# Optimization experiments

Measured on AMD Instinct MI355X. Metric: run time of the kernel, lower is better.

## Reference

```python
import jax, jax.numpy as jnp
import numpy as np

D_MODEL = 768
NUM_HEADS = 12
D_K = D_MODEL // NUM_HEADS


def setup_inputs() -> dict:
    key = jax.random.key(0)
    ks = jax.random.split(key, 9)
    B, N, C = 32, 577, D_MODEL
    s = 1.0 / np.sqrt(C)
    x = jax.random.normal(ks[0], (B, N, C), dtype=jnp.float32)
    Wq = jax.random.normal(ks[1], (C, C), dtype=jnp.float32) * s
    bq = jnp.zeros((C,), dtype=jnp.float32)
    Wk = jax.random.normal(ks[2], (C, C), dtype=jnp.float32) * s
    bk = jnp.zeros((C,), dtype=jnp.float32)
    Wv = jax.random.normal(ks[3], (C, C), dtype=jnp.float32) * s
    bv = jnp.zeros((C,), dtype=jnp.float32)
    Wo = jax.random.normal(ks[4], (C, C), dtype=jnp.float32) * s
    bo = jnp.zeros((C,), dtype=jnp.float32)
    return {"x": x, "Wq": Wq, "bq": bq, "Wk": Wk, "bk": bk,
            "Wv": Wv, "bv": bv, "Wo": Wo, "bo": bo}


def reference(x, Wq, bq, Wk, bk, Wv, bv, Wo, bo):
    B, N, C = x.shape
    H, dk = NUM_HEADS, D_K
    # Linear projections (torch Linear: x @ W.T + b)
    q = (x @ Wq.T + bq).reshape(B, N, H, dk).transpose(0, 2, 1, 3)  # [B,H,N,dk]
    k = (x @ Wk.T + bk).reshape(B, N, H, dk).transpose(0, 2, 1, 3)
    v = (x @ Wv.T + bv).reshape(B, N, H, dk).transpose(0, 2, 1, 3)
    scale = 1.0 / jnp.sqrt(jnp.asarray(dk, dtype=x.dtype))
    scores = jnp.einsum('bhnd,bhmd->bhnm', q, k) * scale  # [B,H,N,N]
    attn = jax.nn.softmax(scores, axis=-1)
    out = jnp.einsum('bhnm,bhmd->bhnd', attn, v)  # [B,H,N,dk]
    out = out.transpose(0, 2, 1, 3).reshape(B, N, C)
    return out @ Wo.T + bo
```

## Files before the change

### kernel.cpp

```cpp
#include <hip/hip_runtime.h>
#include <cstdint>
#include <cstddef>

typedef float  f32x4   __attribute__((ext_vector_type(4)));
typedef __bf16 bf16x8  __attribute__((ext_vector_type(8)));
typedef short  short8  __attribute__((ext_vector_type(8)));
typedef short  short4v __attribute__((ext_vector_type(4)));
typedef float  float4v __attribute__((ext_vector_type(4)));

#define DEVI __device__ __forceinline__

constexpr int Bb = 32, Nn = 577, Cc = 768, Hh = 12, DK = 64;
constexpr int Mm   = Bb * Nn;
constexpr int NQKV = 3 * Cc;
constexpr int NKPAD = 640;
constexpr int NT = 10;
#define QSCALE 0.1803368926f

DEVI short f2bf(float f) {
  __bf16 h = (__bf16)f;
  short s;
  __builtin_memcpy(&s, &h, 2);
  return s;
}

DEVI void gload16(const short* g, short* l) {
  __builtin_amdgcn_global_load_lds(
      (const __attribute__((address_space(1))) void*)g,
      (__attribute__((address_space(3))) void*)l, 16, 0, 0);
}

DEVI f32x4 mfma16(bf16x8 a, bf16x8 b, f32x4 c) {
  return __builtin_amdgcn_mfma_f32_16x16x32_bf16(a, b, c, 0, 0, 0);
}

DEVI void remap_grouped(int bid, int nbm, int nbn, int GM, int& bm, int& bn) {
  const int nwg = nbm * nbn;
  const int xcd = bid & 7, j = bid >> 3;
  const int q = nwg >> 3, r = nwg & 7;
  int wg = (xcd < r ? xcd * (q + 1) : r * (q + 1) + (xcd - r) * q) + j;
  const int per = GM * nbn;
  int grp = wg / per;
  int first = grp * GM;
  int sz = min(GM, nbm - first);
  int rem = wg - grp * per;
  bm = first + rem % sz;
  bn = rem / sz;
}


__global__ void k_cvt_all(const float* __restrict__ x,
                          const float* __restrict__ Wq, const float* __restrict__ Wk,
                          const float* __restrict__ Wv, const float* __restrict__ Wo,
                          short* __restrict__ xb, short* __restrict__ wqkv,
                          short* __restrict__ wob) {
  const int NX4   = Mm * Cc / 4;
  const int WSZ4  = Cc * Cc / 4;
  int i = blockIdx.x * 256 + threadIdx.x;
  const float* src;
  short* dst;
  int e;
  if (i < NX4) { src = x; dst = xb; e = i; }
  else {
    int j = i - NX4;
    if (j < WSZ4)          { src = Wq; dst = wqkv;                e = j; }
    else if (j < 2 * WSZ4) { src = Wk; dst = wqkv + WSZ4 * 4;     e = j - WSZ4; }
    else if (j < 3 * WSZ4) { src = Wv; dst = wqkv + 2 * WSZ4 * 4; e = j - 2 * WSZ4; }
    else if (j < 4 * WSZ4) { src = Wo; dst = wob;                 e = j - 3 * WSZ4; }
    else return;
  }
  float4v v = *(const float4v*)(src + (size_t)e * 4);
  short4v o;
#pragma unroll
  for (int t = 0; t < 4; ++t) o[t] = f2bf(v[t]);
  *(short4v*)(dst + (size_t)e * 4) = o;
}

#define WAITV(N) asm volatile("s_waitcnt vmcnt(" #N ")" ::: "memory")

#define GPH(BUF, KK, MH, STAGE, WAIT)                                      \
  {                                                                        \
    const short* Ab_ = Al + (BUF) * 16384;                                 \
    const short* Bb_ = Bl + (BUF) * 16384;                                 \
    bf16x8 af_[4];                                                         \
    _Pragma("unroll")                                                      \
    for (int m_ = 0; m_ < 4; ++m_)                                         \
      af_[m_] = *(const bf16x8*)(Ab_ + (offA[(MH) * 4 + m_] ^ ((KK) * 32))); \
    if ((MH) == 0) {                                                       \
      _Pragma("unroll")                                                    \
      for (int n_ = 0; n_ < 4; ++n_)                                       \
        bfr[n_] = *(const bf16x8*)(Bb_ + (offB[n_] ^ ((KK) * 32)));        \
    }                                                                      \
    STAGE;                                                                 \
    WAIT;                                                                  \
    __builtin_amdgcn_s_barrier();                                          \
    __builtin_amdgcn_s_setprio(1);                                         \
    _Pragma("unroll")                                                      \
    for (int m_ = 0; m_ < 4; ++m_)                                         \
      _Pragma("unroll")                                                    \
      for (int n_ = 0; n_ < 4; ++n_)                                       \
        acc[(MH) * 4 + m_][n_] = mfma16(af_[m_], bfr[n_], acc[(MH) * 4 + m_][n_]); \
    __builtin_amdgcn_s_setprio(0);                                         \
    __builtin_amdgcn_s_barrier();                                          \
  }

DEVI void gemm256b(const short* __restrict__ A, const short* __restrict__ Bm,
                   int arows, int bm, int bn,
                   short* Al, short* Bl, f32x4 acc[8][4]) {
  const int tid = threadIdx.x;
  const int lane = tid & 63, w = tid >> 6;
  const int wm = w >> 2, wn = w & 3;
  const int qi = lane & 15, g = lane >> 4;

#pragma unroll
  for (int m = 0; m < 8; ++m)
#pragma unroll
    for (int n = 0; n < 4; ++n) acc[m][n] = (f32x4)0.0f;

  const int rloc = tid >> 3, c8 = tid & 7;
  const int gswz = (c8 ^ (rloc & 7)) * 8;
  const short* pA[4];
  const short* pB[4];
#pragma unroll
  for (int s = 0; s < 4; ++s) {
    int ra = bm * 256 + s * 64 + rloc; if (ra > arows - 1) ra = arows - 1;
    pA[s] = A  + (size_t)ra * Cc + gswz;
    pB[s] = Bm + (size_t)(bn * 256 + s * 64 + rloc) * Cc + gswz;
  }
  auto stA = [&](int buf, int s, int co) {
    gload16(pA[s] + co, Al + buf * 16384 + s * 4096 + tid * 8);
  };
  auto stB = [&](int buf, int s, int co) {
    gload16(pB[s] + co, Bl + buf * 16384 + s * 4096 + tid * 8);
  };

  int offA[8], offB[4];
#pragma unroll
  for (int m = 0; m < 8; ++m) {
    int r = wm * 128 + m * 16 + qi;
    offA[m] = r * 64 + ((g ^ (r & 7)) * 8);
  }
#pragma unroll
  for (int n = 0; n < 4; ++n) {
    int r = wn * 64 + n * 16 + qi;
    offB[n] = r * 64 + ((g ^ (r & 7)) * 8);
  }
  bf16x8 bfr[4];

  stA(0, 0, 0); stA(0, 1, 0); stA(0, 2, 0); stA(0, 3, 0);
  stB(0, 0, 0); stB(0, 1, 0); stB(0, 2, 0); stB(0, 3, 0);
  stB(1, 0, 64); stB(1, 1, 64);
  WAITV(2);
  __builtin_amdgcn_s_barrier();

#pragma unroll 1
  for (int i = 0; i < 5; ++i) {
    const int cb1  = 64 + 128 * i;
    const int cb0n = cb1 + 64;
    const int cb1n = cb1 + 128;
    GPH(0, 0, 0, (stB(1, 2, cb1),  stB(1, 3, cb1)),  (void)0);
    GPH(0, 0, 1, (stA(1, 0, cb1),  stA(1, 2, cb1)),  (void)0);
    GPH(0, 1, 0, (stA(1, 1, cb1),  stA(1, 3, cb1)),  (void)0);
    GPH(0, 1, 1, (stA(0, 0, cb0n), stA(0, 2, cb0n)), WAITV(4));
    GPH(1, 0, 0, (stA(0, 1, cb0n), stA(0, 3, cb0n)), WAITV(4));
    GPH(1, 0, 1, (stB(0, 0, cb0n), stB(0, 1, cb0n)), (void)0);
    GPH(1, 1, 0, (stB(0, 2, cb0n), stB(0, 3, cb0n)), (void)0);
    GPH(1, 1, 1, (stB(1, 0, cb1n), stB(1, 1, cb1n)), WAITV(2));
  }
  GPH(0, 0, 0, (stB(1, 2, 704), stB(1, 3, 704)), (void)0);
  GPH(0, 0, 1, (stA(1, 0, 704), stA(1, 2, 704)), (void)0);
  GPH(0, 1, 0, (stA(1, 1, 704), stA(1, 3, 704)), (void)0);
  GPH(0, 1, 1, (void)0, WAITV(2));
  GPH(1, 0, 0, (void)0, WAITV(0));
  GPH(1, 0, 1, (void)0, (void)0);
  GPH(1, 1, 0, (void)0, (void)0);
  GPH(1, 1, 1, (void)0, (void)0);
}

__global__ __launch_bounds__(512) void k_gemm_qkv(
    const short* __restrict__ A, const short* __restrict__ Bm,
    const float* __restrict__ bq, const float* __restrict__ bk, const float* __restrict__ bv,
    short* __restrict__ qv, short* __restrict__ kv, short* __restrict__ vv) {
  __shared__ short Al[2 * 16384];
  __shared__ short Bl[2 * 16384];
  int bm, bn;
  remap_grouped((int)blockIdx.x, (Mm + 255) / 256, NQKV / 256, 4, bm, bn);
  f32x4 acc[8][4];
  gemm256b(A, Bm, Mm, bm, bn, Al, Bl, acc);

  const int lane = threadIdx.x & 63, w = threadIdx.x >> 6;
  const int wm = w >> 2, wn = w & 3;
  const int qi = lane & 15, g = lane >> 4;
  const int cb = bn * 256 + wn * 64;
  const int proj = cb / Cc;
  const int within = cb - proj * Cc;
  const float* bias = proj == 0 ? bq : proj == 1 ? bk : bv;
  short* dst = proj == 0 ? qv : proj == 1 ? kv : vv;
  const float sc = proj == 0 ? QSCALE : 1.0f;
  const int hh = within >> 6;
  float bvv[4];
#pragma unroll
  for (int n = 0; n < 4; ++n) bvv[n] = bias[within + n * 16 + qi];
#pragma unroll
  for (int m = 0; m < 8; ++m)
#pragma unroll
    for (int r = 0; r < 4; ++r) {
      int row = bm * 256 + wm * 128 + m * 16 + g * 4 + r;
      if (row < Mm) {
        int b = row / Nn;
        int nn = row - b * Nn;
        size_t base = ((size_t)(b * Hh + hh) * Nn + nn) * DK;
#pragma unroll
        for (int n = 0; n < 4; ++n)
          dst[base + n * 16 + qi] = f2bf((acc[m][n][r] + bvv[n]) * sc);
      }
    }
}

__global__ __launch_bounds__(512) void k_gemm_out(
    const short* __restrict__ A, const short* __restrict__ Bm,
    const float* __restrict__ bo, float* __restrict__ out) {
  __shared__ short Al[2 * 16384];
  __shared__ short Bl[2 * 16384];
  int bm, bn;
  remap_grouped((int)blockIdx.x, (Mm + 255) / 256, Cc / 256, 8, bm, bn);
  f32x4 acc[8][4];
  gemm256b(A, Bm, Mm, bm, bn, Al, Bl, acc);

  const int lane = threadIdx.x & 63, w = threadIdx.x >> 6;
  const int wm = w >> 2, wn = w & 3;
  const int qi = lane & 15, g = lane >> 4;
  const int cb = bn * 256 + wn * 64;
  float bvv[4];
#pragma unroll
  for (int n = 0; n < 4; ++n) bvv[n] = bo[cb + n * 16 + qi];
#pragma unroll
  for (int m = 0; m < 8; ++m)
#pragma unroll
    for (int r = 0; r < 4; ++r) {
      int row = bm * 256 + wm * 128 + m * 16 + g * 4 + r;
      if (row < Mm) {
#pragma unroll
        for (int n = 0; n < 4; ++n)
          out[(size_t)row * Cc + cb + n * 16 + qi] = acc[m][n][r] + bvv[n];
      }
    }
}

__global__ __launch_bounds__(256) void k_transpose_v(const short* __restrict__ v,
                                                     short* __restrict__ vt) {
  __shared__ short t[64 * 72];
  const int bid = blockIdx.x;
  const int ch = bid % NT, bh = bid / NT;
  const int tid = threadIdx.x;
  const short* vb = v + (size_t)bh * Nn * DK;
#pragma unroll
  for (int i = 0; i < 2; ++i) {
    int gi = i * 256 + tid;
    int r = gi >> 3, c = gi & 7;
    int n = ch * 64 + r;
    short8 val;
#pragma unroll
    for (int j = 0; j < 8; ++j) val[j] = 0;
    if (n < Nn) val = *(const short8*)(vb + (size_t)n * DK + c * 8);
    *(short8*)(t + r * 72 + c * 8) = val;
  }
  __syncthreads();
  short* ob = vt + (size_t)bh * DK * NKPAD + ch * 64;
#pragma unroll
  for (int i = 0; i < 2; ++i) {
    int gi = i * 256 + tid;
    int d = gi >> 3, cg = gi & 7;
    short8 o;
#pragma unroll
    for (int j = 0; j < 8; ++j) o[j] = t[(cg * 8 + j) * 72 + d];
    *(short8*)(ob + (size_t)d * NKPAD + cg * 8) = o;
  }
}

__global__ __launch_bounds__(256) void k_attn(const short* __restrict__ q,
                                              const short* __restrict__ k,
                                              const short* __restrict__ vt,
                                              short* __restrict__ ao) {
  __shared__ short Ks[2][64 * 64];
  __shared__ short Vs[2][64 * 64];
  __shared__ short Ps[4][16 * 64];
  int bid = (int)blockIdx.x;
  bid = (bid & 7) * 240 + (bid >> 3);
  const int qtp = bid % 5, bh = bid / 5;
  const int qt0 = qtp * 2;
  const int bb = bh / Hh, hh = bh - bb * Hh;
  const int tid = threadIdx.x, lane = tid & 63, w = tid >> 6;
  const int qi = lane & 15, g = lane >> 4;

  const short* qb  = q  + (size_t)bh * Nn * DK;
  const short* kb  = k  + (size_t)bh * Nn * DK;
  const short* vtb = vt + (size_t)bh * DK * NKPAD;

  const int qrow = qt0 * 64 + w * 16 + qi;
  const bf16x8 qf0a = *(const bf16x8*)(qb + (size_t)qrow * DK + g * 8);
  const bf16x8 qf1a = *(const bf16x8*)(qb + (size_t)qrow * DK + 32 + g * 8);
  const bf16x8 qf0b = *(const bf16x8*)(qb + (size_t)(qrow + 64) * DK + g * 8);
  const bf16x8 qf1b = *(const bf16x8*)(qb + (size_t)(qrow + 64) * DK + 32 + g * 8);

  const int r0 = tid >> 3, cc = tid & 7;
  const int cs0 = (cc ^ (r0 & 7)) * 8;
  const short* kg = kb + r0 * DK + cs0;
  const short* vg = vtb + (size_t)r0 * NKPAD + cs0;
  short* const Kd0 = &Ks[0][w * 512]; short* const Kd1 = &Ks[1][w * 512];
  short* const Vd0 = &Vs[0][w * 512]; short* const Vd1 = &Vs[1][w * 512];

  auto stage = [&](short* Kd, short* Vd) {
    gload16(kg, Kd);          gload16(kg + 2048,  Kd + 2048);
    gload16(vg, Vd);          gload16(vg + 20480, Vd + 2048);
    kg += 4096;               vg += 64;
  };

  const int swq = qi & 7;
  const short* const KF00 = &Ks[0][qi * 64 + ((g    ) ^ swq) * 8];
  const short* const KF01 = &Ks[0][qi * 64 + ((g + 4) ^ swq) * 8];
  const short* const KF10 = &Ks[1][qi * 64 + ((g    ) ^ swq) * 8];
  const short* const KF11 = &Ks[1][qi * 64 + ((g + 4) ^ swq) * 8];
  const short* const VF00 = &Vs[0][qi * 64 + ((g    ) ^ swq) * 8];
  const short* const VF01 = &Vs[0][qi * 64 + ((g + 4) ^ swq) * 8];
  const short* const VF10 = &Vs[1][qi * 64 + ((g    ) ^ swq) * 8];
  const short* const VF11 = &Vs[1][qi * 64 + ((g + 4) ^ swq) * 8];
  short* const PW0 = &Ps[w][qi * 64 + (((0  + g) ^ (swq << 1)) << 2)];
  short* const PW1 = &Ps[w][qi * 64 + (((4  + g) ^ (swq << 1)) << 2)];
  short* const PW2 = &Ps[w][qi * 64 + (((8  + g) ^ (swq << 1)) << 2)];
  short* const PW3 = &Ps[w][qi * 64 + (((12 + g) ^ (swq << 1)) << 2)];
  const short* const PR0 = &Ps[w][qi * 64 + ((g    ) ^ swq) * 8];
  const short* const PR1 = &Ps[w][qi * 64 + ((g + 4) ^ swq) * 8];

  f32x4 accA[4], accB[4];
#pragma unroll
  for (int nd = 0; nd < 4; ++nd) { accA[nd] = (f32x4)0.0f; accB[nd] = (f32x4)0.0f; }
  float lsA = 0.f, lsB = 0.f;

  auto smax = [&](f32x4* s, float& ls, bool last) {
    if (last) {
#pragma unroll
      for (int ni = 0; ni < 4; ++ni)
#pragma unroll
        for (int r = 0; r < 4; ++r)
          if (ni || r) s[ni][r] = -1e30f;
      if (g) s[0][0] = -1e30f;
    }
    float rs = 0.f;
    short4v pk0, pk1, pk2, pk3;
#pragma unroll
    for (int r = 0; r < 4; ++r) { float p = exp2f(s[0][r]); rs += p; pk0[r] = f2bf(p); }
#pragma unroll
    for (int r = 0; r < 4; ++r) { float p = exp2f(s[1][r]); rs += p; pk1[r] = f2bf(p); }
#pragma unroll
    for (int r = 0; r < 4; ++r) { float p = exp2f(s[2][r]); rs += p; pk2[r] = f2bf(p); }
#pragma unroll
    for (int r = 0; r < 4; ++r) { float p = exp2f(s[3][r]); rs += p; pk3[r] = f2bf(p); }
    *(short4v*)PW0 = pk0; *(short4v*)PW1 = pk1;
    *(short4v*)PW2 = pk2; *(short4v*)PW3 = pk3;
    rs += __shfl_xor(rs, 16);
    rs += __shfl_xor(rs, 32);
    ls += rs;
  };

  auto tilestep = [&](const short* Kf0, const short* Kf1,
                      const short* Vf0, const short* Vf1, bool last) {
    f32x4 sA[4], sB[4];
#pragma unroll
    for (int ni = 0; ni < 4; ++ni) { sA[ni] = (f32x4)0.0f; sB[ni] = (f32x4)0.0f; }
    {
      bf16x8 kf[4];
#pragma unroll
      for (int ni = 0; ni < 4; ++ni) kf[ni] = *(const bf16x8*)(Kf0 + ni * 1024);
#pragma unroll
      for (int ni = 0; ni < 4; ++ni) sA[ni] = mfma16(kf[ni], qf0a, sA[ni]);
#pragma unroll
      for (int ni = 0; ni < 4; ++ni) sB[ni] = mfma16(kf[ni], qf0b, sB[ni]);
#pragma unroll
      for (int ni = 0; ni < 4; ++ni) kf[ni] = *(const bf16x8*)(Kf1 + ni * 1024);
#pragma unroll
      for (int ni = 0; ni < 4; ++ni) sA[ni] = mfma16(kf[ni], qf1a, sA[ni]);
#pragma unroll
      for (int ni = 0; ni < 4; ++ni) sB[ni] = mfma16(kf[ni], qf1b, sB[ni]);
    }
    smax(sA, lsA, last);
    bf16x8 paA0 = *(const bf16x8*)PR0;
    bf16x8 paA1 = *(const bf16x8*)PR1;
    smax(sB, lsB, last);
    bf16x8 paB0 = *(const bf16x8*)PR0;
    bf16x8 paB1 = *(const bf16x8*)PR1;
    {
      bf16x8 vf[4];
#pragma unroll
      for (int nd = 0; nd < 4; ++nd) vf[nd] = *(const bf16x8*)(Vf0 + nd * 1024);
#pragma unroll
      for (int nd = 0; nd < 4; ++nd) accA[nd] = mfma16(paA0, vf[nd], accA[nd]);
#pragma unroll
      for (int nd = 0; nd < 4; ++nd) accB[nd] = mfma16(paB0, vf[nd], accB[nd]);
#pragma unroll
      for (int nd = 0; nd < 4; ++nd) vf[nd] = *(const bf16x8*)(Vf1 + nd * 1024);
#pragma unroll
      for (int nd = 0; nd < 4; ++nd) accA[nd] = mfma16(paA1, vf[nd], accA[nd]);
#pragma unroll
      for (int nd = 0; nd < 4; ++nd) accB[nd] = mfma16(paB1, vf[nd], accB[nd]);
    }
  };

  stage(Kd0, Vd0);
  __syncthreads();
#pragma unroll 1
  for (int t2 = 0; t2 < 5; ++t2) {
    stage(Kd1, Vd1);
    tilestep(KF00, KF01, VF00, VF01, false);
    __syncthreads();
    if (t2 < 4) {
      stage(Kd0, Vd0);
      tilestep(KF10, KF11, VF10, VF11, false);
      __syncthreads();
    }
  }
  tilestep(KF10, KF11, VF10, VF11, true);

  auto epi = [&](f32x4* accd, float ls, int qt) {
    float ls4[4];
#pragma unroll
    for (int r = 0; r < 4; ++r) ls4[r] = __shfl(ls, (g << 2) + r);
#pragma unroll
    for (int r = 0; r < 4; ++r) {
      int qr = qt * 64 + w * 16 + (g << 2) + r;
      if (qr < Nn) {
        float inv = 1.0f / ls4[r];
        size_t base = ((size_t)(bb * Nn + qr)) * Cc + hh * DK;
#pragma unroll
        for (int nd = 0; nd < 4; ++nd)
          ao[base + nd * 16 + qi] = f2bf(accd[nd][r] * inv);
      }
    }
  };
  epi(accA, lsA, qt0);
  epi(accB, lsB, qt0 + 1);
}


extern "C" void kernel_launch(void* const* d_in, const int* in_sizes, int n_in,
                              void* d_out, int out_size, void* d_ws, size_t ws_size,
                              hipStream_t stream) {
  const float* x  = (const float*)d_in[0];
  const float* Wq = (const float*)d_in[1];
  const float* bq = (const float*)d_in[2];
  const float* Wk = (const float*)d_in[3];
  const float* bk = (const float*)d_in[4];
  const float* Wv = (const float*)d_in[5];
  const float* bv = (const float*)d_in[6];
  const float* Wo = (const float*)d_in[7];
  const float* bo = (const float*)d_in[8];
  float* out = (float*)d_out;

  char* ws = (char*)d_ws;
  size_t off = 0;
  auto alloc = [&](size_t bytes) {
    char* p = ws + off;
    off += (bytes + 255) & ~(size_t)255;
    return p;
  };
  short* xb   = (short*)alloc((size_t)Mm * Cc * 2);
  short* wqkv = (short*)alloc((size_t)NQKV * Cc * 2);
  short* wob  = (short*)alloc((size_t)Cc * Cc * 2);
  short* qb   = (short*)alloc((size_t)Bb * Hh * Nn * DK * 2);
  short* kb   = (short*)alloc((size_t)Bb * Hh * Nn * DK * 2);
  short* vb   = (short*)alloc((size_t)Bb * Hh * Nn * DK * 2);
  short* vtb  = (short*)alloc((size_t)Bb * Hh * DK * NKPAD * 2);
  short* aob  = xb;

  const int NCVT = Mm * Cc / 4 + Cc * Cc;
  k_cvt_all<<<(NCVT + 255) / 256, 256, 0, stream>>>(x, Wq, Wk, Wv, Wo, xb, wqkv, wob);

  const int nbm = (Mm + 255) / 256;
  k_gemm_qkv<<<nbm * (NQKV / 256), 512, 0, stream>>>(xb, wqkv, bq, bk, bv, qb, kb, vb);

  k_transpose_v<<<Bb * Hh * NT, 256, 0, stream>>>(vb, vtb);

  k_attn<<<Bb * Hh * 5, 256, 0, stream>>>(qb, kb, vtb, aob);

  k_gemm_out<<<nbm * (Cc / 256), 512, 0, stream>>>(aob, wob, bo, out);
}
```

Before: 212.5 us.

## Trim last attention tile, use native exp2, grid-stride conversion kernel

The final 577th key tile now uses a specialized path that computes only the one valid 16-key MFMA block instead of a full 64-key tile, zeroing the rest of P. exp2f is replaced with the hardware exp2 intrinsic, which skips range/denormal handling. The conversion kernel becomes a grid-stride loop with a fixed 4096-block grid instead of one thread per float4. The intrinsic exp2 may be slightly less accurate, and the fixed grid changes how the conversion work is spread across CUs.

```diff
diff --git a/kernel.cpp b/kernel.cpp
--- a/kernel.cpp
+++ b/kernel.cpp
@@ -23,6 +23,8 @@
   __builtin_memcpy(&s, &h, 2);
   return s;
 }
+
+DEVI float fexp2(float x) { return __builtin_amdgcn_exp2f(x); }
 
 DEVI void gload16(const short* g, short* l) {
   __builtin_amdgcn_global_load_lds(
@@ -56,24 +58,25 @@
                           short* __restrict__ wob) {
   const int NX4   = Mm * Cc / 4;
   const int WSZ4  = Cc * Cc / 4;
-  int i = blockIdx.x * 256 + threadIdx.x;
-  const float* src;
-  short* dst;
-  int e;
-  if (i < NX4) { src = x; dst = xb; e = i; }
-  else {
-    int j = i - NX4;
-    if (j < WSZ4)          { src = Wq; dst = wqkv;                e = j; }
-    else if (j < 2 * WSZ4) { src = Wk; dst = wqkv + WSZ4 * 4;     e = j - WSZ4; }
-    else if (j < 3 * WSZ4) { src = Wv; dst = wqkv + 2 * WSZ4 * 4; e = j - 2 * WSZ4; }
-    else if (j < 4 * WSZ4) { src = Wo; dst = wob;                 e = j - 3 * WSZ4; }
-    else return;
-  }
-  float4v v = *(const float4v*)(src + (size_t)e * 4);
-  short4v o;
-#pragma unroll
-  for (int t = 0; t < 4; ++t) o[t] = f2bf(v[t]);
-  *(short4v*)(dst + (size_t)e * 4) = o;
+  const int NTOT  = NX4 + 4 * WSZ4;
+  for (int i = blockIdx.x * 256 + threadIdx.x; i < NTOT; i += gridDim.x * 256) {
+    const float* src;
+    short* dst;
+    int e;
+    if (i < NX4) { src = x; dst = xb; e = i; }
+    else {
+      int j = i - NX4;
+      if (j < WSZ4)          { src = Wq; dst = wqkv;                e = j; }
+      else if (j < 2 * WSZ4) { src = Wk; dst = wqkv + WSZ4 * 4;     e = j - WSZ4; }
+      else if (j < 3 * WSZ4) { src = Wv; dst = wqkv + 2 * WSZ4 * 4; e = j - 2 * WSZ4; }
+      else                   { src = Wo; dst = wob;                 e = j - 3 * WSZ4; }
+    }
+    float4v v = *(const float4v*)(src + (size_t)e * 4);
+    short4v o;
+#pragma unroll
+    for (int t = 0; t < 4; ++t) o[t] = f2bf(v[t]);
+    *(short4v*)(dst + (size_t)e * 4) = o;
+  }
 }
 
 #define WAITV(N) asm volatile("s_waitcnt vmcnt(" #N ")" ::: "memory")
@@ -337,25 +340,17 @@
   for (int nd = 0; nd < 4; ++nd) { accA[nd] = (f32x4)0.0f; accB[nd] = (f32x4)0.0f; }
   float lsA = 0.f, lsB = 0.f;
 
-  auto smax = [&](f32x4* s, float& ls, bool last) {
-    if (last) {
-#pragma unroll
-      for (int ni = 0; ni < 4; ++ni)
-#pragma unroll
-        for (int r = 0; r < 4; ++r)
-          if (ni || r) s[ni][r] = -1e30f;
-      if (g) s[0][0] = -1e30f;
-    }
+  auto smax = [&](f32x4* s, float& ls) {
     float rs = 0.f;
     short4v pk0, pk1, pk2, pk3;
 #pragma unroll
-    for (int r = 0; r < 4; ++r) { float p = exp2f(s[0][r]); rs += p; pk0[r] = f2bf(p); }
-#pragma unroll
-    for (int r = 0; r < 4; ++r) { float p = exp2f(s[1][r]); rs += p; pk1[r] = f2bf(p); }
-#pragma unroll
-    for (int r = 0; r < 4; ++r) { float p = exp2f(s[2][r]); rs += p; pk2[r] = f2bf(p); }
-#pragma unroll
-    for (int r = 0; r < 4; ++r) { float p = exp2f(s[3][r]); rs += p; pk3[r] = f2bf(p); }
+    for (int r = 0; r < 4; ++r) { float p = fexp2(s[0][r]); rs += p; pk0[r] = f2bf(p); }
+#pragma unroll
+    for (int r = 0; r < 4; ++r) { float p = fexp2(s[1][r]); rs += p; pk1[r] = f2bf(p); }
+#pragma unroll
+    for (int r = 0; r < 4; ++r) { float p = fexp2(s[2][r]); rs += p; pk2[r] = f2bf(p); }
+#pragma unroll
+    for (int r = 0; r < 4; ++r) { float p = fexp2(s[3][r]); rs += p; pk3[r] = f2bf(p); }
     *(short4v*)PW0 = pk0; *(short4v*)PW1 = pk1;
     *(short4v*)PW2 = pk2; *(short4v*)PW3 = pk3;
     rs += __shfl_xor(rs, 16);
@@ -364,7 +359,7 @@
   };
 
   auto tilestep = [&](const short* Kf0, const short* Kf1,
-                      const short* Vf0, const short* Vf1, bool last) {
+                      const short* Vf0, const short* Vf1) {
     f32x4 sA[4], sB[4];
 #pragma unroll
     for (int ni = 0; ni < 4; ++ni) { sA[ni] = (f32x4)0.0f; sB[ni] = (f32x4)0.0f; }
@@ -383,10 +378,10 @@
 #pragma unroll
       for (int ni = 0; ni < 4; ++ni) sB[ni] = mfma16(kf[ni], qf1b, sB[ni]);
     }
-    smax(sA, lsA, last);
+    smax(sA, lsA);
     bf16x8 paA0 = *(const bf16x8*)PR0;
     bf16x8 paA1 = *(const bf16x8*)PR1;
-    smax(sB, lsB, last);
+    smax(sB, lsB);
     bf16x8 paB0 = *(const bf16x8*)PR0;
     bf16x8 paB1 = *(const bf16x8*)PR1;
     {
@@ -404,6 +399,35 @@
 #pragma unroll
       for (int nd = 0; nd < 4; ++nd) accB[nd] = mfma16(paB1, vf[nd], accB[nd]);
     }
+  };
+
+  auto lasttile = [&](const short* Kf0, const short* Kf1,
+                      const short* Vf0) {
+    auto one = [&](const bf16x8& qf0, const bf16x8& qf1, f32x4* accd, float& ls) {
+      f32x4 s0 = (f32x4)0.0f;
+      s0 = mfma16(*(const bf16x8*)(Kf0), qf0, s0);
+      s0 = mfma16(*(const bf16x8*)(Kf1), qf1, s0);
+      float rs = 0.f;
+      short4v pk0, pkz;
+#pragma unroll
+      for (int r = 0; r < 4; ++r) {
+        float sv = (g == 0 && r == 0) ? s0[r] : -1e30f;
+        float p = fexp2(sv);
+        rs += p;
+        pk0[r] = f2bf(p);
+        pkz[r] = 0;
+      }
+      *(short4v*)PW0 = pk0; *(short4v*)PW1 = pkz;
+      rs += __shfl_xor(rs, 16);
+      rs += __shfl_xor(rs, 32);
+      ls += rs;
+      bf16x8 pa0 = *(const bf16x8*)PR0;
+#pragma unroll
+      for (int nd = 0; nd < 4; ++nd)
+        accd[nd] = mfma16(pa0, *(const bf16x8*)(Vf0 + nd * 1024), accd[nd]);
+    };
+    one(qf0a, qf1a, accA, lsA);
+    one(qf0b, qf1b, accB, lsB);
   };
 
   stage(Kd0, Vd0);
@@ -411,15 +435,15 @@
 #pragma unroll 1
   for (int t2 = 0; t2 < 5; ++t2) {
     stage(Kd1, Vd1);
-    tilestep(KF00, KF01, VF00, VF01, false);
+    tilestep(KF00, KF01, VF00, VF01);
     __syncthreads();
     if (t2 < 4) {
       stage(Kd0, Vd0);
-      tilestep(KF10, KF11, VF10, VF11, false);
+      tilestep(KF10, KF11, VF10, VF11);
       __syncthreads();
     }
   }
-  tilestep(KF10, KF11, VF10, VF11, true);
+  lasttile(KF10, KF11, VF10);
 
   auto epi = [&](f32x4* accd, float ls, int qt) {
     float ls4[4];
@@ -472,8 +496,7 @@
   short* vtb  = (short*)alloc((size_t)Bb * Hh * DK * NKPAD * 2);
   short* aob  = xb;
 
-  const int NCVT = Mm * Cc / 4 + Cc * Cc;
-  k_cvt_all<<<(NCVT + 255) / 256, 256, 0, stream>>>(x, Wq, Wk, Wv, Wo, xb, wqkv, wob);
+  k_cvt_all<<<4096, 256, 0, stream>>>(x, Wq, Wk, Wv, Wo, xb, wqkv, wob);
 
   const int nbm = (Mm + 255) / 256;
   k_gemm_qkv<<<nbm * (NQKV / 256), 512, 0, stream>>>(xb, wqkv, bq, bk, bv, qb, kb, vb);
```

After: 199.7 us. 1.06x faster.
